# Optimization experiments

Measured on AMD Instinct MI355X. Metric: run time of the kernel, lower is better.

The kernel has to match this reference:

```python
import jax, jax.numpy as jnp
import numpy as np

B, C, H, W = 2, 64, 128, 128
KH = KW = 3
K = KH * KW
PAD = 1


def conv(x, w, b, pad):
    out = jax.lax.conv_general_dilated(
        x, w, window_strides=(1, 1), padding=[(pad, pad), (pad, pad)],
        dimension_numbers=("NCHW", "OIHW", "NCHW"))
    return out + b[None, :, None, None]


def leaky_relu(x, slope=0.2):
    return jnp.where(x >= 0, x, slope * x)


def deform_conv(img, offset, mask, w, b):
    # img: [B,C,Hi,Wi]; offset: [B,2K,H,W] (dy,dx interleaved per tap); mask: [B,K,H,W]
    Bb, Ci, Hi, Wi = img.shape
    Ho, Wo = offset.shape[2], offset.shape[3]
    off = offset.reshape(Bb, K, 2, Ho, Wo)
    dy, dx = off[:, :, 0], off[:, :, 1]
    ki, kj = jnp.meshgrid(jnp.arange(KH), jnp.arange(KW), indexing="ij")
    ki = ki.reshape(K).astype(img.dtype)
    kj = kj.reshape(K).astype(img.dtype)
    base_h = (jnp.arange(Ho) - PAD).astype(img.dtype)
    base_w = (jnp.arange(Wo) - PAD).astype(img.dtype)
    ys = base_h[None, None, :, None] + ki[None, :, None, None] + dy  # [B,K,Ho,Wo]
    xs = base_w[None, None, None, :] + kj[None, :, None, None] + dx

    y0 = jnp.floor(ys)
    x0 = jnp.floor(xs)
    ty = ys - y0
    tx = xs - x0
    y0i = y0.astype(jnp.int32)
    x0i = x0.astype(jnp.int32)
    flat = img.reshape(Bb, Ci, Hi * Wi)

    def corner(yi, xi, wgt):
        valid = (yi >= 0) & (yi < Hi) & (xi >= 0) & (xi < Wi)
        yc = jnp.clip(yi, 0, Hi - 1)
        xc = jnp.clip(xi, 0, Wi - 1)
        idx = (yc * Wi + xc).reshape(Bb, 1, -1)
        v = jnp.take_along_axis(flat, jnp.broadcast_to(idx, (Bb, Ci, idx.shape[-1])), axis=2)
        v = v.reshape(Bb, Ci, K, Ho, Wo)
        return v * (wgt * valid.astype(img.dtype))[:, None]

    samp = (corner(y0i, x0i, (1 - ty) * (1 - tx))
            + corner(y0i, x0i + 1, (1 - ty) * tx)
            + corner(y0i + 1, x0i, ty * (1 - tx))
            + corner(y0i + 1, x0i + 1, ty * tx))  # [B,C,K,Ho,Wo]
    out = jnp.einsum("ock,bckhw->bohw", w.reshape(w.shape[0], Ci, K), samp * mask[:, None])
    return out + b[None, :, None, None]


def setup_inputs() -> dict:
    key = jax.random.key(0)
    ks = jax.random.split(key, 8)
    s = 0.05  # keep predicted offsets in a realistic few-pixel range
    return {
        "x": jax.random.normal(ks[0], (B, C, H, W), jnp.float32),
        "y": jax.random.normal(ks[1], (B, C, H, W), jnp.float32),
        "w0": jax.random.normal(ks[2], (C, C, 1, 1), jnp.float32) * s,
        "b0": jnp.zeros((C,), jnp.float32),
        "w_om": jax.random.normal(ks[3], (3 * K, 2 * C, KH, KW), jnp.float32) * s,
        "b_om": jnp.zeros((3 * K,), jnp.float32),
        "w_dc": jax.random.normal(ks[4], (C, C, KH, KW), jnp.float32) * s,
        "b_dc": jnp.zeros((C,), jnp.float32),
        "w1": jax.random.normal(ks[5], (C, C, KH, KW), jnp.float32) * s,
        "b1": jnp.zeros((C,), jnp.float32),
        "w2": jax.random.normal(ks[6], (C, C, KH, KW), jnp.float32) * s,
        "b2": jnp.zeros((C,), jnp.float32),
    }


def reference(x, y, w0, b0, w_om, b_om, w_dc, b_dc, w1, b1, w2, b2):
    x0 = conv(x, w0, b0, pad=0)  # 1x1 projection
    om = conv(jnp.concatenate([x0, y], axis=1), w_om, b_om, pad=PAD)
    offset = om[:, : 2 * K]
    mask = 2.0 * jax.nn.sigmoid(om[:, 2 * K :])
    out = x0 + deform_conv(y, offset, mask, w_dc, b_dc)
    return conv(leaky_relu(conv(out, w1, b1, pad=PAD)), w2, b2, pad=PAD) + out
```

## Files before the change

### kernel.cpp

```cpp
#include <hip/hip_runtime.h>
#include <hip/hip_bf16.h>
#include <math.h>

#define BB 2
#define CCH 64
#define HH 128
#define WWD 128
#define HWv (HH*WWD)
#define KK 9
#define KSTEP 18
#define OMKS 36
#define TCOLS 34
#define CSTR 72
#define CSTR2 136
#define DROW 584

typedef __attribute__((ext_vector_type(8))) short bf16x8;
typedef __attribute__((ext_vector_type(4))) float f32x4;
typedef unsigned short u16;
typedef unsigned int u32;

__device__ inline u16 f2bf(float f) {
  __hip_bfloat16 h = __float2bfloat16(f);
  return *reinterpret_cast<u16*>(&h);
}
__device__ inline u32 f2bf2(float lo, float hi) {
  return ((u32)f2bf(hi) << 16) | (u32)f2bf(lo);
}
__device__ inline float bfLO(u32 v) { return __uint_as_float(v << 16); }
__device__ inline float bfHI(u32 v) { return __uint_as_float(v & 0xffff0000u); }
__device__ inline float bf2f(u16 v) { return __uint_as_float((u32)v << 16); }

__global__ __launch_bounds__(256) void pack_all_k(
    const float* __restrict__ w_dc, const float* __restrict__ w1,
    const float* __restrict__ w2, const float* __restrict__ w_om,
    const float* __restrict__ w0, u16* __restrict__ pk_dc,
    u16* __restrict__ pk_w1, u16* __restrict__ pk_w2,
    u16* __restrict__ pk_om, u16* __restrict__ pk_0) {
  int blk = blockIdx.x;
  int tid = threadIdx.x;
  if (blk < 432) {
    const float* w = blk < 144 ? w_dc : (blk < 288 ? w1 : w2);
    u16* dst = blk < 144 ? pk_dc : (blk < 288 ? pk_w1 : pk_w2);
    int idx = (blk % 144) * 256 + tid;
    int j = idx & 7, l = (idx >> 3) & 63;
    int s = (idx >> 9) % 18, q = idx / 9216;
    int co = q * 16 + (l & 15);
    int kp = s * 32 + (l >> 4) * 8 + j;
    dst[idx] = f2bf(w[(co * 64 + (kp & 63)) * 9 + (kp >> 6)]);
  } else if (blk < 576) {
    int idx = (blk - 432) * 256 + tid;
    int j = idx & 7, l = (idx >> 3) & 63;
    int s = (idx >> 9) % 36, q = idx / 18432;
    int co = q * 16 + (l & 15);
    int kp = s * 32 + (l >> 4) * 8 + j;
    pk_om[idx] = (co < 27)
        ? f2bf(w_om[(co * 128 + (kp & 127)) * 9 + (kp >> 7)]) : (u16)0;
  } else {
    int idx = (blk - 576) * 256 + tid;
    int j = idx & 7, l = (idx >> 3) & 63;
    int s = (idx >> 9) & 1, q = idx / 1024;
    int co = q * 16 + (l & 15);
    int k = s * 32 + (l >> 4) * 8 + j;
    pk_0[idx] = f2bf(w0[co * 64 + k]);
  }
}

__global__ __launch_bounds__(256) void conv1x1y_k(const float* __restrict__ x,
    const float* __restrict__ y, const u16* __restrict__ wpack,
    const float* __restrict__ b0, u16* __restrict__ x0bf,
    u16* __restrict__ yt) {
  #define S1ROW 72
  __shared__ __align__(16) float smem[64 * 65];
  u16* samp1 = (u16*)smem;
  int tid = threadIdx.x;
  int lane = tid & 63, q = tid >> 6;
  int pixbase = blockIdx.x * 64;
  int hwb = pixbase & (HWv - 1);
  int b = pixbase >> 14;

  {
    const float* src = y + (size_t)b * CCH * HWv;
    #pragma unroll
    for (int i = 0; i < 16; i++) {
      int ci = i * 4 + q;
      smem[ci * 65 + lane] = src[(size_t)ci * HWv + hwb + lane];
    }
    __syncthreads();
    u32* dst32 = (u32*)(yt + ((size_t)b * HWv + hwb) * 64);
    int lane2 = tid & 31, rr = tid >> 5;
    #pragma unroll
    for (int i = 0; i < 8; i++) {
      int row = i * 8 + rr;
      dst32[row * 32 + lane2] = f2bf2(smem[(2 * lane2) * 65 + row],
                                      smem[(2 * lane2 + 1) * 65 + row]);
    }
    __syncthreads();
  }

  {
    u16 tmp[16];
    #pragma unroll
    for (int i = 0; i < 16; i++) {
      int ci = q * 16 + i;
      tmp[i] = f2bf(x[((size_t)b * CCH + ci) * HWv + hwb + lane]);
    }
    #pragma unroll
    for (int i = 0; i < 2; i++)
      *(bf16x8*)(samp1 + lane * S1ROW + q * 16 + i * 8) = *(bf16x8*)(tmp + i * 8);
  }
  __syncthreads();
  f32x4 acc[4] = {{0,0,0,0},{0,0,0,0},{0,0,0,0},{0,0,0,0}};
  int g = lane >> 4;
  const bf16x8* bp = (const bf16x8*)wpack + (size_t)(q * 2) * 64 + lane;
  #pragma unroll
  for (int s = 0; s < 2; s++) {
    bf16x8 bf = bp[(size_t)s * 64];
    #pragma unroll
    for (int t = 0; t < 4; t++) {
      bf16x8 a = *(const bf16x8*)(samp1 + (t * 16 + (lane & 15)) * S1ROW + g * 8 + s * 32);
      acc[t] = __builtin_amdgcn_mfma_f32_16x16x32_bf16(a, bf, acc[t], 0, 0, 0);
    }
  }
  int co = q * 16 + (lane & 15);
  float bv = b0[co];
  u16* dst = x0bf + ((size_t)b * HWv + hwb + g * 4) * 64 + co;
  #pragma unroll
  for (int t = 0; t < 4; t++)
    #pragma unroll
    for (int r = 0; r < 4; r++)
      dst[(size_t)(t * 16 + r) * 64] = f2bf(acc[t][r] + bv);
}

__global__ __launch_bounds__(512) void omd_k(const u16* __restrict__ x0bf,
    const u16* __restrict__ yt, const u16* __restrict__ pk_om,
    const u16* __restrict__ pk_dc, const float* __restrict__ b_om,
    const float* __restrict__ b_dc, u16* __restrict__ ob) {
  __shared__ __align__(16) u16 A[18688];
  __shared__ __align__(16) int prm[288][8];
  __shared__ __align__(16) float omv[64 * 28];
  u32* A32 = (u32*)A;
  u32* dsamp32 = (u32*)A;
  u16* dsamp = A;
  int tid = threadIdx.x;
  int lane = tid & 63, q = tid >> 6;
  int blk = blockIdx.x;
  int wq = blk & 3, rp = (blk >> 2) & 63, b = blk >> 8;
  int h0 = rp * 2, wb = wq * 32;
  const u32* x0b32 = (const u32*)x0bf + (size_t)b * HWv * 32;
  const u32* yt32  = (const u32*)yt + (size_t)b * HWv * 32;

  {
    int lane2 = tid & 31, g16 = tid >> 5;
    int cofs = lane2 * 2;
    const u32* srcb = (lane2 < 16) ? (x0b32 + cofs) : (yt32 + cofs - 32);
    #pragma unroll
    for (int i = 0; i < 9; i++) {
      int u = g16 + 16 * i;
      if (u < 4 * TCOLS) {
        int r = u / TCOLS, c = u % TCOLS;
        int hh = h0 - 1 + r, ww = wb - 1 + c;
        uint2 v = {0u, 0u};
        if ((unsigned)hh < HH && (unsigned)ww < WWD)
          v = *(const uint2*)(srcb + (size_t)(hh * WWD + ww) * 32);
        *(uint2*)(A32 + u * (CSTR2 / 2) + cofs) = v;
      }
    }
  }
  __syncthreads();

  {
    int r = q & 1, cg = (q >> 1) & 1, cohalf = q >> 2;
    f32x4 acc = {0.f, 0.f, 0.f, 0.f};
    const bf16x8* bp = (const bf16x8*)pk_om + (size_t)(cohalf * OMKS) * 64 + lane;
    #pragma unroll
    for (int s = 0; s < OMKS; s++) {
      int kk = s >> 2;
      int addr = ((r + kk / 3) * TCOLS + cg * 16 + (lane & 15) + (kk % 3)) * CSTR2
                 + (s & 3) * 32 + (lane >> 4) * 8;
      bf16x8 a = *(const bf16x8*)(A + addr);
      acc = __builtin_amdgcn_mfma_f32_16x16x32_bf16(a, bp[(size_t)s * 64], acc, 0, 0, 0);
    }
    int co = cohalf * 16 + (lane & 15);
    if (co < 27) {
      float bv = b_om[co];
      int px = r * 32 + cg * 16 + (lane >> 4) * 4;
      #pragma unroll
      for (int j = 0; j < 4; j++)
        omv[(px + j) * 28 + co] = acc[j] + bv;
    }
  }
  __syncthreads();

  for (int h2 = 0; h2 < 2; h2++) {
    if (tid < 32 * KK) {
      int pl = tid / KK, k = tid % KK;
      const float* omp = omv + (h2 * 32 + pl) * 28;
      float dy = omp[2 * k], dx = omp[2 * k + 1];
      float mk = 2.f / (1.f + expf(-omp[18 + k]));
      float ys = (float)(h0 + h2 - 1 + k / 3) + dy;
      float xs = (float)(wb + pl - 1 + k % 3) + dx;
      float y0f = floorf(ys), x0f = floorf(xs);
      float ty = ys - y0f, tx = xs - x0f;
      int yi = (int)y0f, xi = (int)x0f;
      bool y0v = (unsigned)yi < HH, y1v = (unsigned)(yi + 1) < HH;
      bool x0v = (unsigned)xi < WWD, x1v = (unsigned)(xi + 1) < WWD;
      float w00 = (1.f - ty) * (1.f - tx) * mk * ((y0v && x0v) ? 1.f : 0.f);
      float w01 = (1.f - ty) * tx * mk * ((y0v && x1v) ? 1.f : 0.f);
      float w10 = ty * (1.f - tx) * mk * ((y1v && x0v) ? 1.f : 0.f);
      float w11 = ty * tx * mk * ((y1v && x1v) ? 1.f : 0.f);
      int* p = prm[tid];
      *(int4*)p = make_int4(min(max(yi, 0), HH - 1) * (WWD * 32),
                            min(max(yi + 1, 0), HH - 1) * (WWD * 32),
                            min(max(xi, 0), WWD - 1) * 32,
                            min(max(xi + 1, 0), WWD - 1) * 32);
      *(int4*)(p + 4) = make_int4(__float_as_int(w00), __float_as_int(w01),
                                  __float_as_int(w10), __float_as_int(w11));
    }
    __syncthreads();
    {
      int lane4 = tid & 15, g16 = tid >> 4;
      const u32* ytb = yt32 + lane4 * 2;
      #pragma unroll
      for (int i = 0; i < 9; i++) {
        int u = g16 + 32 * i;
        int k = u % 9, pix = u / 9;
        int4 pa = *(const int4*)prm[u];
        int4 pb = *(const int4*)(prm[u] + 4);
        uint2 v00 = *(const uint2*)(ytb + pa.x + pa.z);
        uint2 v01 = *(const uint2*)(ytb + pa.x + pa.w);
        uint2 v10 = *(const uint2*)(ytb + pa.y + pa.z);
        uint2 v11 = *(const uint2*)(ytb + pa.y + pa.w);
        float w00 = __int_as_float(pb.x), w01 = __int_as_float(pb.y);
        float w10 = __int_as_float(pb.z), w11 = __int_as_float(pb.w);
        float a0 = fmaf(bfLO(v00.x), w00, fmaf(bfLO(v01.x), w01,
                   fmaf(bfLO(v10.x), w10, bfLO(v11.x) * w11)));
        float a1 = fmaf(bfHI(v00.x), w00, fmaf(bfHI(v01.x), w01,
                   fmaf(bfHI(v10.x), w10, bfHI(v11.x) * w11)));
        float a2 = fmaf(bfLO(v00.y), w00, fmaf(bfLO(v01.y), w01,
                   fmaf(bfLO(v10.y), w10, bfLO(v11.y) * w11)));
        float a3 = fmaf(bfHI(v00.y), w00, fmaf(bfHI(v01.y), w01,
                   fmaf(bfHI(v10.y), w10, bfHI(v11.y) * w11)));
        uint2 o = {f2bf2(a0, a1), f2bf2(a2, a3)};
        *(uint2*)(dsamp32 + pix * (DROW / 2) + k * 32 + lane4 * 2) = o;
      }
    }
    __syncthreads();
    {
      int qq = q & 3, pxg = q >> 2;
      f32x4 acc = {0.f, 0.f, 0.f, 0.f};
      const u16* arow = dsamp + (pxg * 16 + (lane & 15)) * DROW + (lane >> 4) * 8;
      const bf16x8* bp = (const bf16x8*)pk_dc + (size_t)(qq * KSTEP) * 64 + lane;
      #pragma unroll
      for (int s = 0; s < KSTEP; s++) {
        bf16x8 a = *(const bf16x8*)(arow + s * 32);
        acc = __builtin_amdgcn_mfma_f32_16x16x32_bf16(a, bp[(size_t)s * 64], acc, 0, 0, 0);
      }
      int co = qq * 16 + (lane & 15);
      int px = pxg * 16 + (lane >> 4) * 4;
      float bv = b_dc[co];
      size_t obase = ((size_t)b * HWv + (h0 + h2) * WWD + wb + px) * 64 + co;
      #pragma unroll
      for (int j = 0; j < 4; j++)
        ob[obase + (size_t)j * 64] =
            f2bf(acc[j] + bv + bf2f(x0bf[obase + (size_t)j * 64]));
    }
    __syncthreads();
  }
}

__global__ __launch_bounds__(512) void rconv12_k(const u16* __restrict__ ob,
    const u16* __restrict__ pk_w1, const u16* __restrict__ pk_w2,
    const float* __restrict__ b1, const float* __restrict__ b2,
    float* __restrict__ outp) {
  #define R2COLS 36
  __shared__ __align__(16) u16 stage[6 * R2COLS * CSTR];
  __shared__ __align__(16) u16 zlds[144 * CSTR];
  u32* stage32 = (u32*)stage;
  int tid = threadIdx.x;
  int lane = tid & 63, q = tid >> 6;
  int blk = blockIdx.x;
  int wq = blk & 3, rp = (blk >> 2) & 63, b = blk >> 8;
  int h0 = rp * 2, wb = wq * 32;

  {
    int lane4 = tid & 15, g16 = tid >> 4;
    const u32* inb = (const u32*)ob + (size_t)b * HWv * 32 + lane4 * 2;
    #pragma unroll
    for (int i = 0; i < 7; i++) {
      int u = g16 + 32 * i;
      if (u < 6 * R2COLS) {
        int r = u / R2COLS, c = u % R2COLS;
        int hh = h0 - 2 + r, ww = wb - 2 + c;
        uint2 v = {0u, 0u};
        if ((unsigned)hh < HH && (unsigned)ww < WWD)
          v = *(const uint2*)(inb + (size_t)(hh * WWD + ww) * 32);
        *(uint2*)(stage32 + u * (CSTR / 2) + lane4 * 2) = v;
      }
    }
  }
  __syncthreads();

  #pragma unroll
  for (int t = 0; t < 5; t++) {
    int task = q + 8 * t;
    if (task < 36) {
      int g = task >> 2, coq = task & 3;
      int p = g * 16 + (lane & 15);
      if (p > 135) p = 135;
      int r1 = p / 34, c1 = p % 34;
      f32x4 acc = {0.f, 0.f, 0.f, 0.f};
      const bf16x8* bp = (const bf16x8*)pk_w1 + (size_t)(coq * KSTEP) * 64 + lane;
      #pragma unroll
      for (int s = 0; s < KSTEP; s++) {
        int kk = s >> 1;
        int addr = ((r1 + kk / 3) * R2COLS + c1 + kk % 3) * CSTR
                   + (s & 1) * 32 + (lane >> 4) * 8;
        bf16x8 a = *(const bf16x8*)(stage + addr);
        acc = __builtin_amdgcn_mfma_f32_16x16x32_bf16(a, bp[(size_t)s * 64], acc, 0, 0, 0);
      }
      int co = coq * 16 + (lane & 15);
      float bv = b1[co];
      int prow = g * 16 + (lane >> 4) * 4;
      #pragma unroll
      for (int j = 0; j < 4; j++) {
        int pp = prow + j;
        int rr = pp / 34, cc = pp % 34;
        bool inimg = ((unsigned)(h0 - 1 + rr) < HH) && ((unsigned)(wb - 1 + cc) < WWD);
        float v = acc[j] + bv;
        v = v >= 0.f ? v : 0.2f * v;
        zlds[pp * CSTR + co] = inimg ? f2bf(v) : (u16)0;
      }
    }
  }
  __syncthreads();

  int r = q & 1, cg = (q >> 1) & 1, copair = q >> 2;
  f32x4 acc2[2] = {{0,0,0,0},{0,0,0,0}};
  const bf16x8* bp2 = (const bf16x8*)pk_w2 + (size_t)(copair * 2 * KSTEP) * 64 + lane;
  #pragma unroll
  for (int s = 0; s < KSTEP; s++) {
    int kk = s >> 1;
    int p = (r + kk / 3) * 34 + cg * 16 + (lane & 15) + (kk % 3);
    int addr = p * CSTR + (s & 1) * 32 + (lane >> 4) * 8;
    bf16x8 a = *(const bf16x8*)(zlds + addr);
    acc2[0] = __builtin_amdgcn_mfma_f32_16x16x32_bf16(a, bp2[(size_t)s * 64], acc2[0], 0, 0, 0);
    acc2[1] = __builtin_amdgcn_mfma_f32_16x16x32_bf16(a, bp2[(size_t)(KSTEP + s) * 64], acc2[1], 0, 0, 0);
  }
  __syncthreads();

  float* ot = (float*)zlds;
  int pxc = cg * 16 + (lane >> 4) * 4;
  #pragma unroll
  for (int t = 0; t < 2; t++) {
    int co = copair * 32 + t * 16 + (lane & 15);
    float bv = b2[co];
    #pragma unroll
    for (int j = 0; j < 4; j++) {
      int c = pxc + j;
      u16 resv = stage[((r + 2) * R2COLS + c + 2) * CSTR + co];
      ot[co * 72 + r * 36 + c] = acc2[t][j] + bv + bf2f(resv);
    }
  }
  __syncthreads();
  int co = tid >> 3, seg = tid & 7;
  int r2 = seg >> 2, c8 = (seg & 3) * 8;
  const float4* src4 = (const float4*)(ot + co * 72 + r2 * 36 + c8);
  float4 v0 = src4[0], v1 = src4[1];
  float* dst = outp + ((size_t)b * CCH + co) * HWv + (h0 + r2) * WWD + wb + c8;
  *(float4*)dst = v0;
  *(float4*)(dst + 4) = v1;
}

extern "C" void kernel_launch(void* const* d_in, const int* in_sizes, int n_in,
                              void* d_out, int out_size, void* d_ws, size_t ws_size,
                              hipStream_t stream) {
  const float* x    = (const float*)d_in[0];
  const float* y    = (const float*)d_in[1];
  const float* w0   = (const float*)d_in[2];
  const float* b0   = (const float*)d_in[3];
  const float* w_om = (const float*)d_in[4];
  const float* b_om = (const float*)d_in[5];
  const float* w_dc = (const float*)d_in[6];
  const float* b_dc = (const float*)d_in[7];
  const float* w1   = (const float*)d_in[8];
  const float* b1   = (const float*)d_in[9];
  const float* w2   = (const float*)d_in[10];
  const float* b2   = (const float*)d_in[11];
  float* out = (float*)d_out;

  const size_t NFULL = (size_t)BB * CCH * HWv;
  const size_t NPACK = 4 * KSTEP * 64 * 8;
  const size_t NPACKOM = 2 * OMKS * 64 * 8;
  u16* x0bf = (u16*)d_ws;
  u16* ob   = x0bf + NFULL;
  u16* yt   = ob + NFULL;
  u16* pk_dc = yt + NFULL;
  u16* pk_w1 = pk_dc + NPACK;
  u16* pk_w2 = pk_w1 + NPACK;
  u16* pk_om = pk_w2 + NPACK;
  u16* pk_0  = pk_om + NPACKOM;

  const int NB = (int)((size_t)BB * HWv / 64);

  pack_all_k<<<592, 256, 0, stream>>>(w_dc, w1, w2, w_om, w0,
                                      pk_dc, pk_w1, pk_w2, pk_om, pk_0);
  conv1x1y_k<<<NB, 256, 0, stream>>>(x, y, pk_0, b0, x0bf, yt);
  omd_k<<<NB, 512, 0, stream>>>(x0bf, yt, pk_om, pk_dc, b_om, b_dc, ob);
  rconv12_k<<<NB, 512, 0, stream>>>(ob, pk_w1, pk_w2, b1, b2, out);
}
```

Baseline: 60.43 us.

## Merge weight packing into 1x1 conv kernel, remap blocks, hoist sampling params

Removes the separate weight-packing launch by appending packing blocks to the 1x1-conv/transposition kernel and loading w0 fragments directly into registers there. The omd and rconv kernels remap block indices so consecutive blocks land on different rows/batches, likely to spread work across XCDs and improve L2 locality. The deformable sampling parameters for both rows are computed in one pass before sampling, which removes a barrier per row at the cost of a larger shared-memory parameter array that may reduce occupancy.

```diff
diff --git a/kernel.cpp b/kernel.cpp
--- a/kernel.cpp
+++ b/kernel.cpp
@@ -31,53 +31,57 @@
 __device__ inline float bfHI(u32 v) { return __uint_as_float(v & 0xffff0000u); }
 __device__ inline float bf2f(u16 v) { return __uint_as_float((u32)v << 16); }
 
-__global__ __launch_bounds__(256) void pack_all_k(
-    const float* __restrict__ w_dc, const float* __restrict__ w1,
-    const float* __restrict__ w2, const float* __restrict__ w_om,
-    const float* __restrict__ w0, u16* __restrict__ pk_dc,
-    u16* __restrict__ pk_w1, u16* __restrict__ pk_w2,
-    u16* __restrict__ pk_om, u16* __restrict__ pk_0) {
-  int blk = blockIdx.x;
-  int tid = threadIdx.x;
-  if (blk < 432) {
-    const float* w = blk < 144 ? w_dc : (blk < 288 ? w1 : w2);
-    u16* dst = blk < 144 ? pk_dc : (blk < 288 ? pk_w1 : pk_w2);
-    int idx = (blk % 144) * 256 + tid;
-    int j = idx & 7, l = (idx >> 3) & 63;
-    int s = (idx >> 9) % 18, q = idx / 9216;
-    int co = q * 16 + (l & 15);
-    int kp = s * 32 + (l >> 4) * 8 + j;
-    dst[idx] = f2bf(w[(co * 64 + (kp & 63)) * 9 + (kp >> 6)]);
-  } else if (blk < 576) {
-    int idx = (blk - 432) * 256 + tid;
-    int j = idx & 7, l = (idx >> 3) & 63;
-    int s = (idx >> 9) % 36, q = idx / 18432;
-    int co = q * 16 + (l & 15);
-    int kp = s * 32 + (l >> 4) * 8 + j;
-    pk_om[idx] = (co < 27)
-        ? f2bf(w_om[(co * 128 + (kp & 127)) * 9 + (kp >> 7)]) : (u16)0;
-  } else {
-    int idx = (blk - 576) * 256 + tid;
-    int j = idx & 7, l = (idx >> 3) & 63;
-    int s = (idx >> 9) & 1, q = idx / 1024;
-    int co = q * 16 + (l & 15);
-    int k = s * 32 + (l >> 4) * 8 + j;
-    pk_0[idx] = f2bf(w0[co * 64 + k]);
-  }
-}
-
-__global__ __launch_bounds__(256) void conv1x1y_k(const float* __restrict__ x,
-    const float* __restrict__ y, const u16* __restrict__ wpack,
-    const float* __restrict__ b0, u16* __restrict__ x0bf,
-    u16* __restrict__ yt) {
+__global__ __launch_bounds__(256) void c1y_pack_k(const float* __restrict__ x,
+    const float* __restrict__ y, const float* __restrict__ w0,
+    const float* __restrict__ b0, const float* __restrict__ w_dc,
+    const float* __restrict__ w1, const float* __restrict__ w2,
+    const float* __restrict__ w_om, u16* __restrict__ x0bf,
+    u16* __restrict__ yt, u16* __restrict__ pk_dc, u16* __restrict__ pk_w1,
+    u16* __restrict__ pk_w2, u16* __restrict__ pk_om) {
   #define S1ROW 72
   __shared__ __align__(16) float smem[64 * 65];
+  int tid = threadIdx.x;
+
+  if (blockIdx.x >= 512) {
+    int blk = blockIdx.x - 512;
+    if (blk < 432) {
+      const float* w = blk < 144 ? w_dc : (blk < 288 ? w1 : w2);
+      u16* dst = blk < 144 ? pk_dc : (blk < 288 ? pk_w1 : pk_w2);
+      int idx = (blk % 144) * 256 + tid;
+      int j = idx & 7, l = (idx >> 3) & 63;
+      int s = (idx >> 9) % 18, q = idx / 9216;
+      int co = q * 16 + (l & 15);
+      int kp = s * 32 + (l >> 4) * 8 + j;
+      dst[idx] = f2bf(w[(co * 64 + (kp & 63)) * 9 + (kp >> 6)]);
+    } else {
+      int idx = (blk - 432) * 256 + tid;
+      int j = idx & 7, l = (idx >> 3) & 63;
+      int s = (idx >> 9) % 36, q = idx / 18432;
+      int co = q * 16 + (l & 15);
+      int kp = s * 32 + (l >> 4) * 8 + j;
+      pk_om[idx] = (co < 27)
+          ? f2bf(w_om[(co * 128 + (kp & 127)) * 9 + (kp >> 7)]) : (u16)0;
+    }
+    return;
+  }
+
   u16* samp1 = (u16*)smem;
-  int tid = threadIdx.x;
   int lane = tid & 63, q = tid >> 6;
   int pixbase = blockIdx.x * 64;
   int hwb = pixbase & (HWv - 1);
   int b = pixbase >> 14;
+  int co = q * 16 + (lane & 15);
+  int g = lane >> 4;
+
+  bf16x8 wfrag[2];
+  #pragma unroll
+  for (int s = 0; s < 2; s++) {
+    const float* wp = w0 + co * 64 + s * 32 + g * 8;
+    u16 tw[8];
+    #pragma unroll
+    for (int j = 0; j < 8; j++) tw[j] = f2bf(wp[j]);
+    wfrag[s] = *(bf16x8*)tw;
+  }
 
   {
     const float* src = y + (size_t)b * CCH * HWv;
@@ -111,18 +115,14 @@
   }
   __syncthreads();
   f32x4 acc[4] = {{0,0,0,0},{0,0,0,0},{0,0,0,0},{0,0,0,0}};
-  int g = lane >> 4;
-  const bf16x8* bp = (const bf16x8*)wpack + (size_t)(q * 2) * 64 + lane;
   #pragma unroll
   for (int s = 0; s < 2; s++) {
-    bf16x8 bf = bp[(size_t)s * 64];
     #pragma unroll
     for (int t = 0; t < 4; t++) {
       bf16x8 a = *(const bf16x8*)(samp1 + (t * 16 + (lane & 15)) * S1ROW + g * 8 + s * 32);
-      acc[t] = __builtin_amdgcn_mfma_f32_16x16x32_bf16(a, bf, acc[t], 0, 0, 0);
-    }
-  }
-  int co = q * 16 + (lane & 15);
+      acc[t] = __builtin_amdgcn_mfma_f32_16x16x32_bf16(a, wfrag[s], acc[t], 0, 0, 0);
+    }
+  }
   float bv = b0[co];
   u16* dst = x0bf + ((size_t)b * HWv + hwb + g * 4) * 64 + co;
   #pragma unroll
@@ -137,14 +137,14 @@
     const u16* __restrict__ pk_dc, const float* __restrict__ b_om,
     const float* __restrict__ b_dc, u16* __restrict__ ob) {
   __shared__ __align__(16) u16 A[18688];
-  __shared__ __align__(16) int prm[288][8];
+  __shared__ __align__(16) int prm[576][8];
   __shared__ __align__(16) float omv[64 * 28];
   u32* A32 = (u32*)A;
   u32* dsamp32 = (u32*)A;
   u16* dsamp = A;
   int tid = threadIdx.x;
   int lane = tid & 63, q = tid >> 6;
-  int blk = blockIdx.x;
+  int blk = (blockIdx.x & 7) * 64 + (blockIdx.x >> 3);
   int wq = blk & 3, rp = (blk >> 2) & 63, b = blk >> 8;
   int h0 = rp * 2, wb = wq * 32;
   const u32* x0b32 = (const u32*)x0bf + (size_t)b * HWv * 32;
@@ -192,14 +192,17 @@
   }
   __syncthreads();
 
-  for (int h2 = 0; h2 < 2; h2++) {
-    if (tid < 32 * KK) {
-      int pl = tid / KK, k = tid % KK;
-      const float* omp = omv + (h2 * 32 + pl) * 28;
+  #pragma unroll
+  for (int t = 0; t < 2; t++) {
+    int u = tid + 512 * t;
+    if (u < 576) {
+      int pl = u / KK, k = u % KK;
+      int r2 = pl >> 5, cl = pl & 31;
+      const float* omp = omv + pl * 28;
       float dy = omp[2 * k], dx = omp[2 * k + 1];
       float mk = 2.f / (1.f + expf(-omp[18 + k]));
-      float ys = (float)(h0 + h2 - 1 + k / 3) + dy;
-      float xs = (float)(wb + pl - 1 + k % 3) + dx;
+      float ys = (float)(h0 + r2 - 1 + k / 3) + dy;
+      float xs = (float)(wb + cl - 1 + k % 3) + dx;
       float y0f = floorf(ys), x0f = floorf(xs);
       float ty = ys - y0f, tx = xs - x0f;
       int yi = (int)y0f, xi = (int)x0f;
@@ -209,7 +212,7 @@
       float w01 = (1.f - ty) * tx * mk * ((y0v && x1v) ? 1.f : 0.f);
       float w10 = ty * (1.f - tx) * mk * ((y1v && x0v) ? 1.f : 0.f);
       float w11 = ty * tx * mk * ((y1v && x1v) ? 1.f : 0.f);
-      int* p = prm[tid];
+      int* p = prm[u];
       *(int4*)p = make_int4(min(max(yi, 0), HH - 1) * (WWD * 32),
                             min(max(yi + 1, 0), HH - 1) * (WWD * 32),
                             min(max(xi, 0), WWD - 1) * 32,
@@ -217,7 +220,11 @@
       *(int4*)(p + 4) = make_int4(__float_as_int(w00), __float_as_int(w01),
                                   __float_as_int(w10), __float_as_int(w11));
     }
-    __syncthreads();
+  }
+  __syncthreads();
+
+  #pragma unroll
+  for (int h2 = 0; h2 < 2; h2++) {
     {
       int lane4 = tid & 15, g16 = tid >> 4;
       const u32* ytb = yt32 + lane4 * 2;
@@ -225,8 +232,9 @@
       for (int i = 0; i < 9; i++) {
         int u = g16 + 32 * i;
         int k = u % 9, pix = u / 9;
-        int4 pa = *(const int4*)prm[u];
-        int4 pb = *(const int4*)(prm[u] + 4);
+        const int* pp = prm[h2 * 288 + u];
+        int4 pa = *(const int4*)pp;
+        int4 pb = *(const int4*)(pp + 4);
         uint2 v00 = *(const uint2*)(ytb + pa.x + pa.z);
         uint2 v01 = *(const uint2*)(ytb + pa.x + pa.w);
         uint2 v10 = *(const uint2*)(ytb + pa.y + pa.z);
@@ -265,7 +273,7 @@
         ob[obase + (size_t)j * 64] =
             f2bf(acc[j] + bv + bf2f(x0bf[obase + (size_t)j * 64]));
     }
-    __syncthreads();
+    if (h2 == 0) __syncthreads();
   }
 }
 
@@ -279,7 +287,7 @@
   u32* stage32 = (u32*)stage;
   int tid = threadIdx.x;
   int lane = tid & 63, q = tid >> 6;
-  int blk = blockIdx.x;
+  int blk = (blockIdx.x & 7) * 64 + (blockIdx.x >> 3);
   int wq = blk & 3, rp = (blk >> 2) & 63, b = blk >> 8;
   int h0 = rp * 2, wb = wq * 32;
 
@@ -391,7 +399,6 @@
 
   const size_t NFULL = (size_t)BB * CCH * HWv;
   const size_t NPACK = 4 * KSTEP * 64 * 8;
-  const size_t NPACKOM = 2 * OMKS * 64 * 8;
   u16* x0bf = (u16*)d_ws;
   u16* ob   = x0bf + NFULL;
   u16* yt   = ob + NFULL;
@@ -399,13 +406,11 @@
   u16* pk_w1 = pk_dc + NPACK;
   u16* pk_w2 = pk_w1 + NPACK;
   u16* pk_om = pk_w2 + NPACK;
-  u16* pk_0  = pk_om + NPACKOM;
 
   const int NB = (int)((size_t)BB * HWv / 64);
 
-  pack_all_k<<<592, 256, 0, stream>>>(w_dc, w1, w2, w_om, w0,
-                                      pk_dc, pk_w1, pk_w2, pk_om, pk_0);
-  conv1x1y_k<<<NB, 256, 0, stream>>>(x, y, pk_0, b0, x0bf, yt);
+  c1y_pack_k<<<NB + 576, 256, 0, stream>>>(x, y, w0, b0, w_dc, w1, w2, w_om,
+                                           x0bf, yt, pk_dc, pk_w1, pk_w2, pk_om);
   omd_k<<<NB, 512, 0, stream>>>(x0bf, yt, pk_om, pk_dc, b_om, b_dc, ob);
   rconv12_k<<<NB, 512, 0, stream>>>(ob, pk_w1, pk_w2, b1, b2, out);
 }
```

After: 52.99 us. 1.14x faster.
